# Optimization experiments

Measured on AMD Instinct MI355X. Metric: run time of the kernel, lower is better.

## Reference

```python
import jax, jax.numpy as jnp
import numpy as np

S0, P0 = 4096, 64      # level0 segments, points per level0 segment
S1, P1 = 1024, 256     # level1 superpoints, points per level1 segment
C = 128                # feature dim
KNN = 3                # K (neighbor_range=1 -> 3 candidates)
N = S0 * P0


def setup_inputs() -> dict:
    key = jax.random.key(0)
    ks = jax.random.split(key, 8)
    return {
        "sp_center_feat": jax.random.normal(ks[0], (S1, C), jnp.float32),
        "sp_center_coord": jax.random.normal(ks[1], (S1, 3), jnp.float32),
        "rawPoint_feat": jax.random.normal(ks[2], (N, C), jnp.float32),
        "hilbert_feat_coord": jax.random.normal(ks[3], (N, 3), jnp.float32),
        "points_feat": jax.random.normal(ks[4], (S0, P0, C), jnp.float32),
        "points_coord": jax.random.normal(ks[5], (S0, P0, 3), jnp.float32),
        "level0_to_level1_indices": jnp.sort(jax.random.randint(ks[6], (S0,), 0, S1)).astype(jnp.int64),
        "num_segments0": S0,
        "points_per_segment0": P0,
        "num_segments1": S1,
        "points_per_segment1": P1,
        "K": KNN,
    }


def reference(sp_center_feat, sp_center_coord, rawPoint_feat, hilbert_feat_coord,
              points_feat, points_coord, level0_to_level1_indices,
              num_segments0, points_per_segment0, num_segments1, points_per_segment1, K):
    # --- neighbor superpoint candidates (neighbor_range = 1) ---
    offsets = jnp.arange(-1, 2)                                        # [3]
    nb = jnp.clip(jnp.arange(num_segments0)[:, None] + offsets[None, :], 0, num_segments0 - 1)  # [S0,3]
    sp_idx = level0_to_level1_indices[nb]                              # [S0,3]
    nb_feat = sp_center_feat[sp_idx]                                   # [S0,3,C]
    nb_coord = sp_center_coord[sp_idx]                                 # [S0,3,3]

    # --- cdist + topk (smallest K) ---
    diff = points_coord[:, :, None, :] - nb_coord[:, None, :, :]       # [S0,P0,3,3]
    dist = jnp.sqrt(jnp.maximum(jnp.sum(diff * diff, axis=-1), 0.0))   # [S0,P0,3]
    _, knn_idx = jax.lax.top_k(-dist, K)                               # [S0,P0,K], ascending distance

    # --- gather neighbor feats, dot-product similarity, softmax, argmax ---
    b = jnp.arange(num_segments0)[:, None, None]
    knn_sp_feats = nb_feat[b, knn_idx]                                 # [S0,P0,K,C]
    sim = jnp.einsum('spc,spkc->spk', points_feat, knn_sp_feats)       # [S0,P0,K]
    sim = jax.nn.softmax(sim, axis=-1)
    max_idx = jnp.argmax(sim, axis=-1)                                 # [S0,P0]

    # --- map winning neighbor slot -> superpoint id ---
    sp_knn = sp_idx[b, knn_idx]                                        # [S0,P0,K]
    assigned = jnp.take_along_axis(sp_knn, max_idx[..., None], axis=2)[..., 0]  # [S0,P0]
    point_assignments = assigned.reshape(-1)                           # [N]

    # cross_attention_update_sp is empty -> sp_center_feat passes through unchanged

    # --- scatter-mean: new superpoint centers ---
    seg_sum = jax.ops.segment_sum(hilbert_feat_coord, point_assignments, num_segments=num_segments1)
    counts = jax.ops.segment_sum(jnp.ones((point_assignments.shape[0],), hilbert_feat_coord.dtype),
                                 point_assignments, num_segments=num_segments1)
    new_sp_center_coord = seg_sum / jnp.maximum(counts, 1.0)[:, None]  # [S1,3]

    feat_dim = rawPoint_feat.shape[-1]
    hilbert_feat_level1 = rawPoint_feat.reshape(num_segments1, points_per_segment1, feat_dim)
    points_feat_out = rawPoint_feat.reshape(num_segments0, points_per_segment0, feat_dim)

    return (point_assignments, sp_center_feat, new_sp_center_coord, points_feat_out, hilbert_feat_level1)
```

## Files before the change

### kernel.cpp

```cpp
#include <hip/hip_runtime.h>

#define S0 4096
#define P0 64
#define S1 1024
#define P1 256
#define C  128
#define N_PTS (S0 * P0)

#define SEG_PER_BLK 4
#define PT_PER_BLK  256
#define CHUNK       32
#define PSTRIDE     36

__global__ __launch_bounds__(256) void assign_kernel(
    const float* __restrict__ sp_feat,
    const float* __restrict__ pts_feat,
    const float* __restrict__ hilb,
    const int*   __restrict__ l01,
    float* __restrict__ out_assign,
    float* __restrict__ ws_sum,
    float* __restrict__ ws_cnt)
{
    __shared__ float pt_lds[PT_PER_BLK * PSTRIDE];
    __shared__ float cf_lds[6 * C];
    __shared__ float lsum[6][3];
    __shared__ float lcnt[6];
    __shared__ int   lidx[6];

    const int tid    = threadIdx.x;
    const int blk    = blockIdx.x;
    const int s_base = blk * SEG_PER_BLK;

    if (tid < 6) {
        int nb = s_base - 1 + tid;
        nb = nb < 0 ? 0 : (nb >= S0 ? S0 - 1 : nb);
        lidx[tid] = l01[nb];
        lcnt[tid] = 0.0f;
    }
    if (tid < 18) lsum[tid / 3][tid % 3] = 0.0f;
    __syncthreads();

    for (int i = tid; i < 6 * C; i += 256)
        cf_lds[i] = sp_feat[(size_t)lidx[i >> 7] * C + (i & (C - 1))];

    const size_t blk_base = (size_t)blk * PT_PER_BLK * C;
    const int    si       = tid >> 6;
    float d0 = 0.f, d1 = 0.f, d2 = 0.f;

    for (int ch = 0; ch < C; ch += CHUNK) {
        #pragma unroll
        for (int it = 0; it < 8; ++it) {
            int i  = tid + it * 256;
            int pt = i >> 3, q = i & 7;
            float4 v = *reinterpret_cast<const float4*>(
                pts_feat + blk_base + (size_t)pt * C + ch + q * 4);
            *reinterpret_cast<float4*>(&pt_lds[pt * PSTRIDE + q * 4]) = v;
        }
        __syncthreads();

        const float* prow = &pt_lds[tid * PSTRIDE];
        const float* c0   = &cf_lds[(si + 0) * C + ch];
        const float* c1   = &cf_lds[(si + 1) * C + ch];
        const float* c2   = &cf_lds[(si + 2) * C + ch];
        #pragma unroll
        for (int j = 0; j < CHUNK; j += 4) {
            float4 v  = *reinterpret_cast<const float4*>(prow + j);
            float4 a0 = *reinterpret_cast<const float4*>(c0 + j);
            float4 a1 = *reinterpret_cast<const float4*>(c1 + j);
            float4 a2 = *reinterpret_cast<const float4*>(c2 + j);
            d0 += v.x * a0.x + v.y * a0.y + v.z * a0.z + v.w * a0.w;
            d1 += v.x * a1.x + v.y * a1.y + v.z * a1.z + v.w * a1.w;
            d2 += v.x * a2.x + v.y * a2.y + v.z * a2.z + v.w * a2.w;
        }
        __syncthreads();
    }

    int kb = 0; float best = d0;
    if (d1 > best) { best = d1; kb = 1; }
    if (d2 > best) { best = d2; kb = 2; }
    const int slot = si + kb;
    const int gpt  = blk * PT_PER_BLK + tid;

    out_assign[gpt] = (float)lidx[slot];

    const float hx = hilb[(size_t)gpt * 3 + 0];
    const float hy = hilb[(size_t)gpt * 3 + 1];
    const float hz = hilb[(size_t)gpt * 3 + 2];
    atomicAdd(&lsum[slot][0], hx);
    atomicAdd(&lsum[slot][1], hy);
    atomicAdd(&lsum[slot][2], hz);
    atomicAdd(&lcnt[slot], 1.0f);
    __syncthreads();

    if (tid < 6 && lcnt[tid] > 0.0f) {
        atomicAdd(&ws_cnt[lidx[tid]], lcnt[tid]);
        atomicAdd(&ws_sum[(size_t)lidx[tid] * 3 + 0], lsum[tid][0]);
        atomicAdd(&ws_sum[(size_t)lidx[tid] * 3 + 1], lsum[tid][1]);
        atomicAdd(&ws_sum[(size_t)lidx[tid] * 3 + 2], lsum[tid][2]);
    }
}

__global__ void copy_kernel(const float4* __restrict__ raw,
                            float4* __restrict__ o_pf,
                            float4* __restrict__ o_h1,
                            const float4* __restrict__ spf,
                            float4* __restrict__ o_spf,
                            const float* __restrict__ ws_sum,
                            const float* __restrict__ ws_cnt,
                            float* __restrict__ out_coord)
{
    const long gid = (long)blockIdx.x * blockDim.x + threadIdx.x;
    if (gid < S1 * 3)
        out_coord[gid] = ws_sum[gid] / fmaxf(ws_cnt[gid / 3], 1.0f);

    const long NR = (long)N_PTS * C / 4;
    const long NS = (long)S1 * C / 4;
    for (long i = gid; i < NR; i += (long)gridDim.x * blockDim.x) {
        float4 v = raw[i];
        o_pf[i] = v;
        o_h1[i] = v;
        if (i < NS) o_spf[i] = spf[i];
    }
}

extern "C" void kernel_launch(void* const* d_in, const int* in_sizes, int n_in,
                              void* d_out, int out_size, void* d_ws, size_t ws_size,
                              hipStream_t stream) {
    const float* sp_feat  = (const float*)d_in[0];
    const float* raw      = (const float*)d_in[2];
    const float* hilb     = (const float*)d_in[3];
    const float* pts_feat = (const float*)d_in[4];
    const int*   l01      = (const int*)d_in[6];

    float* out        = (float*)d_out;
    float* out_assign = out;
    float* out_spfeat = out_assign + N_PTS;
    float* out_coord  = out_spfeat + (size_t)S1 * C;
    float* out_pf     = out_coord + (size_t)S1 * 3;
    float* out_h1     = out_pf + (size_t)S0 * P0 * C;

    float* ws_sum = (float*)d_ws;
    float* ws_cnt = ws_sum + (size_t)S1 * 3;

    hipMemsetAsync(d_ws, 0, (size_t)(S1 * 3 + S1) * sizeof(float), stream);

    assign_kernel<<<S0 / SEG_PER_BLK, 256, 0, stream>>>(
        sp_feat, pts_feat, hilb, l01, out_assign, ws_sum, ws_cnt);

    copy_kernel<<<2048, 256, 0, stream>>>(
        (const float4*)raw, (float4*)out_pf, (float4*)out_h1,
        (const float4*)sp_feat, (float4*)out_spfeat,
        ws_sum, ws_cnt, out_coord);
}
```

Measured before the change: 128.9 us.

## Fuse assignment and bulk copy into one kernel, drop LDS staging of point features

Merges the assignment work and the large feature copy into a single launch: the first 1024 blocks do the nearest-superpoint assignment and then join the grid-stride copy, while the remaining blocks only copy. This lets the memory-bound copy overlap the assignment compute and removes one kernel boundary. The assignment also stops staging point features through LDS; each thread now reads its 512-byte row directly from global memory, which is uncoalesced across a wavefront. A small finalize kernel computes the scatter-mean coordinates after the fused kernel.

```diff
diff --git a/kernel.cpp b/kernel.cpp
--- a/kernel.cpp
+++ b/kernel.cpp
@@ -7,63 +7,57 @@
 #define C  128
 #define N_PTS (S0 * P0)
 
-#define SEG_PER_BLK 4
-#define PT_PER_BLK  256
-#define CHUNK       32
-#define PSTRIDE     36
+#define SEG_PER_BLK   4
+#define PT_PER_BLK    256
+#define ASSIGN_BLOCKS (S0 / SEG_PER_BLK)
+#define TOTAL_BLOCKS  2048
 
-__global__ __launch_bounds__(256) void assign_kernel(
+__global__ __launch_bounds__(256) void fused_kernel(
     const float* __restrict__ sp_feat,
     const float* __restrict__ pts_feat,
     const float* __restrict__ hilb,
     const int*   __restrict__ l01,
-    float* __restrict__ out_assign,
-    float* __restrict__ ws_sum,
-    float* __restrict__ ws_cnt)
+    const float4* __restrict__ raw,
+    float*  __restrict__ out_assign,
+    float4* __restrict__ o_pf,
+    float4* __restrict__ o_h1,
+    float4* __restrict__ o_spf,
+    float*  __restrict__ ws_sum,
+    float*  __restrict__ ws_cnt)
 {
-    __shared__ float pt_lds[PT_PER_BLK * PSTRIDE];
     __shared__ float cf_lds[6 * C];
     __shared__ float lsum[6][3];
     __shared__ float lcnt[6];
     __shared__ int   lidx[6];
 
-    const int tid    = threadIdx.x;
-    const int blk    = blockIdx.x;
-    const int s_base = blk * SEG_PER_BLK;
+    const int tid = threadIdx.x;
+    const int blk = blockIdx.x;
 
-    if (tid < 6) {
-        int nb = s_base - 1 + tid;
-        nb = nb < 0 ? 0 : (nb >= S0 ? S0 - 1 : nb);
-        lidx[tid] = l01[nb];
-        lcnt[tid] = 0.0f;
-    }
-    if (tid < 18) lsum[tid / 3][tid % 3] = 0.0f;
-    __syncthreads();
-
-    for (int i = tid; i < 6 * C; i += 256)
-        cf_lds[i] = sp_feat[(size_t)lidx[i >> 7] * C + (i & (C - 1))];
-
-    const size_t blk_base = (size_t)blk * PT_PER_BLK * C;
-    const int    si       = tid >> 6;
-    float d0 = 0.f, d1 = 0.f, d2 = 0.f;
-
-    for (int ch = 0; ch < C; ch += CHUNK) {
-        #pragma unroll
-        for (int it = 0; it < 8; ++it) {
-            int i  = tid + it * 256;
-            int pt = i >> 3, q = i & 7;
-            float4 v = *reinterpret_cast<const float4*>(
-                pts_feat + blk_base + (size_t)pt * C + ch + q * 4);
-            *reinterpret_cast<float4*>(&pt_lds[pt * PSTRIDE + q * 4]) = v;
+    if (blk < ASSIGN_BLOCKS) {
+        const int s_base = blk * SEG_PER_BLK;
+        if (tid < 6) {
+            int nb = s_base - 1 + tid;
+            nb = nb < 0 ? 0 : (nb >= S0 ? S0 - 1 : nb);
+            lidx[tid] = l01[nb];
+            lcnt[tid] = 0.0f;
         }
+        if (tid < 18) lsum[tid / 3][tid % 3] = 0.0f;
         __syncthreads();
 
-        const float* prow = &pt_lds[tid * PSTRIDE];
-        const float* c0   = &cf_lds[(si + 0) * C + ch];
-        const float* c1   = &cf_lds[(si + 1) * C + ch];
-        const float* c2   = &cf_lds[(si + 2) * C + ch];
+        for (int i = tid; i < 6 * C; i += 256)
+            cf_lds[i] = sp_feat[(size_t)lidx[i >> 7] * C + (i & (C - 1))];
+        __syncthreads();
+
+        const int si  = tid >> 6;
+        const int gpt = blk * PT_PER_BLK + tid;
+        const float* prow = pts_feat + (size_t)gpt * C;
+        const float* c0 = &cf_lds[(si + 0) * C];
+        const float* c1 = &cf_lds[(si + 1) * C];
+        const float* c2 = &cf_lds[(si + 2) * C];
+
+        float d0 = 0.f, d1 = 0.f, d2 = 0.f;
         #pragma unroll
-        for (int j = 0; j < CHUNK; j += 4) {
+        for (int j = 0; j < C; j += 4) {
             float4 v  = *reinterpret_cast<const float4*>(prow + j);
             float4 a0 = *reinterpret_cast<const float4*>(c0 + j);
             float4 a1 = *reinterpret_cast<const float4*>(c1 + j);
@@ -72,55 +66,48 @@
             d1 += v.x * a1.x + v.y * a1.y + v.z * a1.z + v.w * a1.w;
             d2 += v.x * a2.x + v.y * a2.y + v.z * a2.z + v.w * a2.w;
         }
+
+        int kb = 0; float best = d0;
+        if (d1 > best) { best = d1; kb = 1; }
+        if (d2 > best) { best = d2; kb = 2; }
+        const int slot = si + kb;
+
+        out_assign[gpt] = (float)lidx[slot];
+
+        atomicAdd(&lsum[slot][0], hilb[(size_t)gpt * 3 + 0]);
+        atomicAdd(&lsum[slot][1], hilb[(size_t)gpt * 3 + 1]);
+        atomicAdd(&lsum[slot][2], hilb[(size_t)gpt * 3 + 2]);
+        atomicAdd(&lcnt[slot], 1.0f);
         __syncthreads();
+
+        if (tid < 6 && lcnt[tid] > 0.0f) {
+            atomicAdd(&ws_cnt[lidx[tid]], lcnt[tid]);
+            atomicAdd(&ws_sum[(size_t)lidx[tid] * 3 + 0], lsum[tid][0]);
+            atomicAdd(&ws_sum[(size_t)lidx[tid] * 3 + 1], lsum[tid][1]);
+            atomicAdd(&ws_sum[(size_t)lidx[tid] * 3 + 2], lsum[tid][2]);
+        }
     }
 
-    int kb = 0; float best = d0;
-    if (d1 > best) { best = d1; kb = 1; }
-    if (d2 > best) { best = d2; kb = 2; }
-    const int slot = si + kb;
-    const int gpt  = blk * PT_PER_BLK + tid;
-
-    out_assign[gpt] = (float)lidx[slot];
-
-    const float hx = hilb[(size_t)gpt * 3 + 0];
-    const float hy = hilb[(size_t)gpt * 3 + 1];
-    const float hz = hilb[(size_t)gpt * 3 + 2];
-    atomicAdd(&lsum[slot][0], hx);
-    atomicAdd(&lsum[slot][1], hy);
-    atomicAdd(&lsum[slot][2], hz);
-    atomicAdd(&lcnt[slot], 1.0f);
-    __syncthreads();
-
-    if (tid < 6 && lcnt[tid] > 0.0f) {
-        atomicAdd(&ws_cnt[lidx[tid]], lcnt[tid]);
-        atomicAdd(&ws_sum[(size_t)lidx[tid] * 3 + 0], lsum[tid][0]);
-        atomicAdd(&ws_sum[(size_t)lidx[tid] * 3 + 1], lsum[tid][1]);
-        atomicAdd(&ws_sum[(size_t)lidx[tid] * 3 + 2], lsum[tid][2]);
+    const long NR = (long)N_PTS * C / 4;
+    const long NS = (long)S1 * C / 4;
+    const long gid    = (long)blk * 256 + tid;
+    const long stride = (long)TOTAL_BLOCKS * 256;
+    const float4* spf4 = (const float4*)sp_feat;
+    for (long i = gid; i < NR; i += stride) {
+        float4 v = raw[i];
+        o_pf[i] = v;
+        o_h1[i] = v;
+        if (i < NS) o_spf[i] = spf4[i];
     }
 }
 
-__global__ void copy_kernel(const float4* __restrict__ raw,
-                            float4* __restrict__ o_pf,
-                            float4* __restrict__ o_h1,
-                            const float4* __restrict__ spf,
-                            float4* __restrict__ o_spf,
-                            const float* __restrict__ ws_sum,
-                            const float* __restrict__ ws_cnt,
-                            float* __restrict__ out_coord)
+__global__ void finalize_kernel(const float* __restrict__ ws_sum,
+                                const float* __restrict__ ws_cnt,
+                                float* __restrict__ out_coord)
 {
-    const long gid = (long)blockIdx.x * blockDim.x + threadIdx.x;
-    if (gid < S1 * 3)
-        out_coord[gid] = ws_sum[gid] / fmaxf(ws_cnt[gid / 3], 1.0f);
-
-    const long NR = (long)N_PTS * C / 4;
-    const long NS = (long)S1 * C / 4;
-    for (long i = gid; i < NR; i += (long)gridDim.x * blockDim.x) {
-        float4 v = raw[i];
-        o_pf[i] = v;
-        o_h1[i] = v;
-        if (i < NS) o_spf[i] = spf[i];
-    }
+    int i = blockIdx.x * blockDim.x + threadIdx.x;
+    if (i >= S1 * 3) return;
+    out_coord[i] = ws_sum[i] / fmaxf(ws_cnt[i / 3], 1.0f);
 }
 
 extern "C" void kernel_launch(void* const* d_in, const int* in_sizes, int n_in,
@@ -144,11 +131,10 @@
 
     hipMemsetAsync(d_ws, 0, (size_t)(S1 * 3 + S1) * sizeof(float), stream);
 
-    assign_kernel<<<S0 / SEG_PER_BLK, 256, 0, stream>>>(
-        sp_feat, pts_feat, hilb, l01, out_assign, ws_sum, ws_cnt);
+    fused_kernel<<<TOTAL_BLOCKS, 256, 0, stream>>>(
+        sp_feat, pts_feat, hilb, l01, (const float4*)raw,
+        out_assign, (float4*)out_pf, (float4*)out_h1, (float4*)out_spfeat,
+        ws_sum, ws_cnt);
 
-    copy_kernel<<<2048, 256, 0, stream>>>(
-        (const float4*)raw, (float4*)out_pf, (float4*)out_h1,
-        (const float4*)sp_feat, (float4*)out_spfeat,
-        ws_sum, ws_cnt, out_coord);
+    finalize_kernel<<<(S1 * 3 + 255) / 256, 256, 0, stream>>>(ws_sum, ws_cnt, out_coord);
 }
```

Result: no change. 128.1 us (-0.6%).
